# Kernel tuning notes

Hardware: AMD Instinct MI355X
Metric: run time of the kernel (lower is better)

## Reference

```python
import jax, jax.numpy as jnp
import numpy as np

VIEW_NUM = 360
CHAN_NUM = 512
BATCH = 2
IMG = 512


def setup_inputs() -> dict:
    key = jax.random.key(0)
    x = jax.random.normal(key, (BATCH, 1, IMG, IMG), dtype=jnp.float32)
    return {"x": x}


def _bilinear_sample_zeros(img, ix, iy):
    """Bilinear sample img (B,1,H,W) at pixel coords ix, iy (H,W), zeros padding.
    Matches F.grid_sample(mode='bilinear', padding_mode='zeros', align_corners=False)."""
    H, W = img.shape[-2], img.shape[-1]
    x0 = jnp.floor(ix)
    y0 = jnp.floor(iy)
    x1 = x0 + 1.0
    y1 = y0 + 1.0
    wx1 = ix - x0
    wx0 = 1.0 - wx1
    wy1 = iy - y0
    wy0 = 1.0 - wy1

    def gather(yy, xx):
        valid = (xx >= 0) & (xx <= W - 1) & (yy >= 0) & (yy <= H - 1)
        xi = jnp.clip(xx, 0, W - 1).astype(jnp.int32)
        yi = jnp.clip(yy, 0, H - 1).astype(jnp.int32)
        # fancy-index over spatial dims -> (B,1,H,W)
        return img[:, :, yi, xi] * valid.astype(img.dtype)

    return (gather(y0, x0) * (wy0 * wx0)
            + gather(y0, x1) * (wy0 * wx1)
            + gather(y1, x0) * (wy1 * wx0)
            + gather(y1, x1) * (wy1 * wx1))


def _fp(x):
    B, C, H, W = x.shape
    # affine_grid base coords, align_corners=False: (2i+1)/N - 1
    bx = (2.0 * jnp.arange(W, dtype=x.dtype) + 1.0) / W - 1.0
    by = (2.0 * jnp.arange(H, dtype=x.dtype) + 1.0) / H - 1.0
    X = bx[None, :]  # (1,W)
    Y = by[:, None]  # (H,1)
    i = jnp.arange(VIEW_NUM, dtype=x.dtype)
    angles = -jnp.pi * (i + 1.0) / VIEW_NUM - jnp.pi
    cosv = jnp.cos(angles)
    sinv = jnp.sin(angles)

    def per_view(carry, cs):
        c, s = cs
        # theta = [[c,-s,0],[s,c,0]]; grid = base @ theta^T
        gx = c * X - s * Y  # (H,W) normalized sample x
        gy = s * X + c * Y  # (H,W) normalized sample y
        # unnormalize (align_corners=False)
        ix = ((gx + 1.0) * W - 1.0) * 0.5
        iy = ((gy + 1.0) * H - 1.0) * 0.5
        samp = _bilinear_sample_zeros(x, ix, iy)  # (B,1,H,W)
        return carry, jnp.sum(samp, axis=2)  # sum over height -> (B,1,W)

    _, cols = jax.lax.scan(per_view, 0, (cosv, sinv))  # (V,B,1,W)
    sino = jnp.transpose(cols, (1, 2, 3, 0)) * 0.5  # (B,1,chanNum,viewNum)
    return sino


def reference(x):
    return _fp(x)
```

## Files before the change

kernel.cpp:

```cpp
#include <hip/hip_runtime.h>

typedef __fp16 h2 __attribute__((ext_vector_type(2)));

constexpr int VIEWS = 360;
constexpr int IMGSZ = 512;
constexpr int WCHUNK = 64;
constexpr int KH = 40;
constexpr int NXF4 = 25;
constexpr int PITCH = 100;
constexpr int MAXNY = 79;
constexpr int LDSDW = PITCH * MAXNY;
constexpr int PW = 712;
constexpr int PH = 704;
constexpr int PAD = 96;

#define ASYNC_CP16(SRC, DST)                                              \
    __builtin_amdgcn_global_load_lds(                                     \
        (const __attribute__((address_space(1))) unsigned*)(SRC),         \
        (__attribute__((address_space(3))) unsigned*)(DST), 16, 0, 0)

__global__ __launch_bounds__(256) void pad_kernel(const float* __restrict__ x,
                                                  unsigned* __restrict__ padq) {
    constexpr int PW4 = PW / 4;
    constexpr int total = PH * PW4;
    int idx = blockIdx.x * 256 + threadIdx.x;
    if (idx >= total) return;
    int py = idx / PW4;
    int px4 = idx - py * PW4;
    int gx = px4 * 4 - PAD;
    int gy = py - PAD;
    const float* img0 = x;
    const float* img1 = x + (size_t)IMGSZ * IMGSZ;
    float4 a = make_float4(0.f, 0.f, 0.f, 0.f);
    float4 bq = a;
    if ((unsigned)gy < (unsigned)IMGSZ && (unsigned)gx < (unsigned)IMGSZ) {
        size_t off = (size_t)gy * IMGSZ + gx;
        a  = *(const float4*)(img0 + off);
        bq = *(const float4*)(img1 + off);
    }
    uint4 d;
    d.x = __builtin_bit_cast(unsigned, __builtin_amdgcn_cvt_pkrtz(a.x, bq.x));
    d.y = __builtin_bit_cast(unsigned, __builtin_amdgcn_cvt_pkrtz(a.y, bq.y));
    d.z = __builtin_bit_cast(unsigned, __builtin_amdgcn_cvt_pkrtz(a.z, bq.z));
    d.w = __builtin_bit_cast(unsigned, __builtin_amdgcn_cvt_pkrtz(a.w, bq.w));
    *(uint4*)&padq[(size_t)idx * 4] = d;
}

__global__ __launch_bounds__(256) void fp_kernel(const unsigned* __restrict__ padq,
                                                 float* __restrict__ out) {
    __shared__ __align__(16) unsigned tileU[LDSDW];

    int blk = blockIdx.x;
    int wc = blk & 7;
    int v = blk >> 3;

    int tid = threadIdx.x;
    int lane = tid & 63;
    int g = tid >> 6;
    int w = wc * WCHUNK + lane;

    double ang = -3.14159265358979323846 * (double)(v + 1) / (double)VIEWS
                 - 3.14159265358979323846;
    float c = (float)cos(ang);
    float s = (float)sin(ang);

    float xw = (float)w + 0.5f - 256.0f;
    float cxw = fmaf(c, xw, 255.5f);
    float sxw = fmaf(s, xw, 255.5f);

    float lo = -1e30f, hi = 1e30f;
    {
        float coef = -s, base = cxw;
        if (fabsf(coef) > 1e-6f) {
            float a = (-1.0f - base) / coef;
            float bq = (512.0f - base) / coef;
            lo = fmaxf(lo, fminf(a, bq));
            hi = fminf(hi, fmaxf(a, bq));
        } else if (!(base > -1.0f && base < 512.0f)) {
            lo = 1e30f; hi = -1e30f;
        }
    }
    {
        float coef = c, base = sxw;
        if (fabsf(coef) > 1e-6f) {
            float a = (-1.0f - base) / coef;
            float bq = (512.0f - base) / coef;
            lo = fmaxf(lo, fminf(a, bq));
            hi = fminf(hi, fmaxf(a, bq));
        } else if (!(base > -1.0f && base < 512.0f)) {
            lo = 1e30f; hi = -1e30f;
        }
    }
    float h0f = fminf(fmaxf(floorf(lo + 255.5f) - 1.0f, 0.0f), 512.0f);
    float h1f = fminf(fmaxf(ceilf(hi + 255.5f) + 1.0f, -1.0f), 511.0f);
    int h0 = (int)h0f;
    int h1 = (int)h1f;

    int bh0 = h0, bh1 = h1;
    #pragma unroll
    for (int m = 1; m < 64; m <<= 1) {
        bh0 = min(bh0, __shfl_xor(bh0, m, 64));
        bh1 = max(bh1, __shfl_xor(bh1, m, 64));
    }

    float xa = (float)(wc * WCHUNK) + 0.5f - 256.0f;
    float xb = xa + 63.0f;

    float acc0 = 0.0f, acc1 = 0.0f;
    float step4x = -4.0f * s;
    float step4y = 4.0f * c;

    for (int hc = bh0; hc <= bh1; hc += KH) {
        int hend = min(hc + KH - 1, bh1);

        float ha = (float)hc - 255.5f;
        float hb = (float)hend - 255.5f;
        float ix00 = c * xa - s * ha, ix01 = c * xa - s * hb;
        float ix10 = c * xb - s * ha, ix11 = c * xb - s * hb;
        float iy00 = s * xa + c * ha, iy01 = s * xa + c * hb;
        float iy10 = s * xb + c * ha, iy11 = s * xb + c * hb;
        float ixmn = fminf(fminf(ix00, ix01), fminf(ix10, ix11)) + 255.5f;
        float iymn = fminf(fminf(iy00, iy01), fminf(iy10, iy11)) + 255.5f;
        float iymx = fmaxf(fmaxf(iy00, iy01), fmaxf(iy10, iy11)) + 255.5f;
        int x_lo = (int)floorf(ixmn) - 1;
        int x_lo4 = x_lo & ~3;
        int y_lo = (int)floorf(iymn) - 1;
        int NY = min((int)floorf(iymx) + 3 - y_lo, MAXNY);
        int total4 = NY * NXF4;
        int nit = (total4 + 255) >> 8;

        __syncthreads();

        {
            const unsigned* pb = padq + (y_lo + PAD) * PW + (x_lo4 + PAD);
            for (int k = 0; k < nit; ++k) {
                int i = (k << 8) + tid;
                if (((k << 8) + (g << 6) + 63) < total4) {
                    int ry = i / NXF4;
                    ASYNC_CP16(pb + 4 * i + (PW - 4 * NXF4) * ry, &tileU[i << 2]);
                } else if (i < total4) {
                    int ry = i / NXF4;
                    uint4 val = *(const uint4*)(pb + 4 * i + (PW - 4 * NXF4) * ry);
                    *(uint4*)&tileU[i << 2] = val;
                }
            }
        }
        asm volatile("s_waitcnt vmcnt(0)" ::: "memory");
        __syncthreads();

        float hh0 = (float)(hc + g) - 255.5f;
        float ixr = fmaf(-s, hh0, cxw) - (float)x_lo4;
        float iyr = fmaf(c, hh0, sxw) - (float)y_lo;
        h2 accp0 = (h2)0.0f;
        h2 accp1 = (h2)0.0f;
        int parity = 0;
        #pragma unroll 8
        for (int h = hc + g; h <= hend; h += 4) {
            float fx = floorf(ixr);
            float fy = floorf(iyr);
            int lx = (int)fx;
            int ly = (int)fy;
            float wx1 = ixr - fx;
            float wy1 = iyr - fy;
            h2 wxs = __builtin_amdgcn_cvt_pkrtz(wx1, wx1);
            h2 wys = __builtin_amdgcn_cvt_pkrtz(wy1, wy1);
            const unsigned* p = tileU + (ly * PITCH + lx);
            h2 t00 = __builtin_bit_cast(h2, p[0]);
            h2 t01 = __builtin_bit_cast(h2, p[1]);
            h2 t10 = __builtin_bit_cast(h2, p[PITCH]);
            h2 t11 = __builtin_bit_cast(h2, p[PITCH + 1]);
            h2 r0 = t00 + (t01 - t00) * wxs;
            h2 r1 = t10 + (t11 - t10) * wxs;
            h2 contrib = r0 + (r1 - r0) * wys;
            if (parity) accp1 += contrib; else accp0 += contrib;
            parity ^= 1;
            ixr += step4x;
            iyr += step4y;
        }
        acc0 += (float)accp0.x + (float)accp1.x;
        acc1 += (float)accp0.y + (float)accp1.y;
    }

    __syncthreads();
    tileU[(g << 6) + lane] = __float_as_uint(acc0);
    tileU[256 + (g << 6) + lane] = __float_as_uint(acc1);
    __syncthreads();
    if (g == 0) {
        float r0 = __uint_as_float(tileU[lane]) + __uint_as_float(tileU[64 + lane]) +
                   __uint_as_float(tileU[128 + lane]) + __uint_as_float(tileU[192 + lane]);
        float r1 = __uint_as_float(tileU[256 + lane]) + __uint_as_float(tileU[320 + lane]) +
                   __uint_as_float(tileU[384 + lane]) + __uint_as_float(tileU[448 + lane]);
        size_t o = (size_t)w * VIEWS + v;
        out[o] = r0 * 0.5f;
        out[(size_t)IMGSZ * VIEWS + o] = r1 * 0.5f;
    }
}

extern "C" void kernel_launch(void* const* d_in, const int* in_sizes, int n_in,
                              void* d_out, int out_size, void* d_ws, size_t ws_size,
                              hipStream_t stream) {
    const float* x = (const float*)d_in[0];
    float* out = (float*)d_out;
    unsigned* padq = (unsigned*)d_ws;

    constexpr int padTotal = PH * (PW / 4);
    pad_kernel<<<(padTotal + 255) / 256, 256, 0, stream>>>(x, padq);

    int nblocks = VIEWS * (IMGSZ / WCHUNK);
    fp_kernel<<<nblocks, 256, 0, stream>>>(padq, out);
}
```

Measured before the change: 165.8 us.

## Enlarge LDS tile to 104 rows with 512 threads and power-of-two pitch

The forward-projection kernel now loads taller image tiles (104 rows per chunk, 128-word pitch, up to 127 tile rows) and runs 512 threads per block, with 8 row phases instead of 4. Tile bounds are updated incrementally rather than recomputed from the four corners each chunk, and address math uses shifts instead of divides. The padded workspace geometry changes to match. This cuts the number of load and sync rounds per block, but the larger LDS footprint (about 65 KB) and bigger blocks can lower occupancy and may load more unused pixels per tile.

```diff
diff --git a/kernel.cpp b/kernel.cpp
--- a/kernel.cpp
+++ b/kernel.cpp
@@ -5,14 +5,15 @@
 constexpr int VIEWS = 360;
 constexpr int IMGSZ = 512;
 constexpr int WCHUNK = 64;
-constexpr int KH = 40;
-constexpr int NXF4 = 25;
-constexpr int PITCH = 100;
-constexpr int MAXNY = 79;
+constexpr int KH = 104;
+constexpr int NPH = 8;
+constexpr int PITCH = 128;
+constexpr int NXF4 = 32;
+constexpr int MAXNY = 127;
 constexpr int LDSDW = PITCH * MAXNY;
-constexpr int PW = 712;
-constexpr int PH = 704;
-constexpr int PAD = 96;
+constexpr int PW = 704;
+constexpr int PH = 705;
+constexpr int PAD = 68;
 
 #define ASYNC_CP16(SRC, DST)                                              \
     __builtin_amdgcn_global_load_lds(                                     \
@@ -46,7 +47,7 @@
     *(uint4*)&padq[(size_t)idx * 4] = d;
 }
 
-__global__ __launch_bounds__(256) void fp_kernel(const unsigned* __restrict__ padq,
+__global__ __launch_bounds__(512) void fp_kernel(const unsigned* __restrict__ padq,
                                                  float* __restrict__ out) {
     __shared__ __align__(16) unsigned tileU[LDSDW];
 
@@ -56,7 +57,7 @@
 
     int tid = threadIdx.x;
     int lane = tid & 63;
-    int g = tid >> 6;
+    int p = tid >> 6;
     int w = wc * WCHUNK + lane;
 
     double ang = -3.14159265358979323846 * (double)(v + 1) / (double)VIEWS
@@ -105,42 +106,55 @@
 
     float xa = (float)(wc * WCHUNK) + 0.5f - 256.0f;
     float xb = xa + 63.0f;
+    float cxa = c * xa, cxb = c * xb;
+    float sxa = s * xa, sxb = s * xb;
+    float xlo_pair = fminf(cxa, cxb);
+    float ylo_pair = fminf(sxa, sxb);
+    float yhi_pair = fmaxf(sxa, sxb);
 
     float acc0 = 0.0f, acc1 = 0.0f;
-    float step4x = -4.0f * s;
-    float step4y = 4.0f * c;
+    float step8x = -8.0f * s;
+    float step8y = 8.0f * c;
+
+    float ixmn = 0.f, iymn = 0.f, iymx = 0.f;
+    bool have = false;
 
     for (int hc = bh0; hc <= bh1; hc += KH) {
         int hend = min(hc + KH - 1, bh1);
 
-        float ha = (float)hc - 255.5f;
-        float hb = (float)hend - 255.5f;
-        float ix00 = c * xa - s * ha, ix01 = c * xa - s * hb;
-        float ix10 = c * xb - s * ha, ix11 = c * xb - s * hb;
-        float iy00 = s * xa + c * ha, iy01 = s * xa + c * hb;
-        float iy10 = s * xb + c * ha, iy11 = s * xb + c * hb;
-        float ixmn = fminf(fminf(ix00, ix01), fminf(ix10, ix11)) + 255.5f;
-        float iymn = fminf(fminf(iy00, iy01), fminf(iy10, iy11)) + 255.5f;
-        float iymx = fmaxf(fmaxf(iy00, iy01), fmaxf(iy10, iy11)) + 255.5f;
-        int x_lo = (int)floorf(ixmn) - 1;
-        int x_lo4 = x_lo & ~3;
+        if (!have || hend != hc + KH - 1) {
+            float ha = (float)hc - 255.5f;
+            float hb = (float)hend - 255.5f;
+            float sha = s * ha, shb = s * hb;
+            float cha = c * ha, chb = c * hb;
+            ixmn = xlo_pair - fmaxf(sha, shb) + 255.5f;
+            iymn = ylo_pair + fminf(cha, chb) + 255.5f;
+            iymx = yhi_pair + fmaxf(cha, chb) + 255.5f;
+        }
+        have = true;
+
+        int x_lo4 = ((int)floorf(ixmn) - 1) & ~3;
         int y_lo = (int)floorf(iymn) - 1;
         int NY = min((int)floorf(iymx) + 3 - y_lo, MAXNY);
-        int total4 = NY * NXF4;
-        int nit = (total4 + 255) >> 8;
+        int total4 = NY << 5;
+        int nit = (total4 + 511) >> 9;
+
+        ixmn -= s * (float)KH;
+        iymn += c * (float)KH;
+        iymx += c * (float)KH;
 
         __syncthreads();
 
         {
             const unsigned* pb = padq + (y_lo + PAD) * PW + (x_lo4 + PAD);
             for (int k = 0; k < nit; ++k) {
-                int i = (k << 8) + tid;
-                if (((k << 8) + (g << 6) + 63) < total4) {
-                    int ry = i / NXF4;
-                    ASYNC_CP16(pb + 4 * i + (PW - 4 * NXF4) * ry, &tileU[i << 2]);
+                int i = (k << 9) + tid;
+                if (((k << 9) + (p << 6) + 63) < total4) {
+                    int ry = i >> 5;
+                    ASYNC_CP16(pb + ((i & 31) << 2) + ry * PW, &tileU[i << 2]);
                 } else if (i < total4) {
-                    int ry = i / NXF4;
-                    uint4 val = *(const uint4*)(pb + 4 * i + (PW - 4 * NXF4) * ry);
+                    int ry = i >> 5;
+                    uint4 val = *(const uint4*)(pb + ((i & 31) << 2) + ry * PW);
                     *(uint4*)&tileU[i << 2] = val;
                 }
             }
@@ -148,14 +162,14 @@
         asm volatile("s_waitcnt vmcnt(0)" ::: "memory");
         __syncthreads();
 
-        float hh0 = (float)(hc + g) - 255.5f;
+        float hh0 = (float)(hc + p) - 255.5f;
         float ixr = fmaf(-s, hh0, cxw) - (float)x_lo4;
         float iyr = fmaf(c, hh0, sxw) - (float)y_lo;
         h2 accp0 = (h2)0.0f;
         h2 accp1 = (h2)0.0f;
         int parity = 0;
         #pragma unroll 8
-        for (int h = hc + g; h <= hend; h += 4) {
+        for (int h = hc + p; h <= hend; h += 8) {
             float fx = floorf(ixr);
             float fy = floorf(iyr);
             int lx = (int)fx;
@@ -164,35 +178,34 @@
             float wy1 = iyr - fy;
             h2 wxs = __builtin_amdgcn_cvt_pkrtz(wx1, wx1);
             h2 wys = __builtin_amdgcn_cvt_pkrtz(wy1, wy1);
-            const unsigned* p = tileU + (ly * PITCH + lx);
-            h2 t00 = __builtin_bit_cast(h2, p[0]);
-            h2 t01 = __builtin_bit_cast(h2, p[1]);
-            h2 t10 = __builtin_bit_cast(h2, p[PITCH]);
-            h2 t11 = __builtin_bit_cast(h2, p[PITCH + 1]);
+            const unsigned* pt = tileU + ((ly << 7) + lx);
+            h2 t00 = __builtin_bit_cast(h2, pt[0]);
+            h2 t01 = __builtin_bit_cast(h2, pt[1]);
+            h2 t10 = __builtin_bit_cast(h2, pt[PITCH]);
+            h2 t11 = __builtin_bit_cast(h2, pt[PITCH + 1]);
             h2 r0 = t00 + (t01 - t00) * wxs;
             h2 r1 = t10 + (t11 - t10) * wxs;
             h2 contrib = r0 + (r1 - r0) * wys;
             if (parity) accp1 += contrib; else accp0 += contrib;
             parity ^= 1;
-            ixr += step4x;
-            iyr += step4y;
+            ixr += step8x;
+            iyr += step8y;
         }
         acc0 += (float)accp0.x + (float)accp1.x;
         acc1 += (float)accp0.y + (float)accp1.y;
     }
 
     __syncthreads();
-    tileU[(g << 6) + lane] = __float_as_uint(acc0);
-    tileU[256 + (g << 6) + lane] = __float_as_uint(acc1);
+    tileU[(p << 6) + lane] = __float_as_uint(acc0);
+    tileU[512 + (p << 6) + lane] = __float_as_uint(acc1);
     __syncthreads();
-    if (g == 0) {
-        float r0 = __uint_as_float(tileU[lane]) + __uint_as_float(tileU[64 + lane]) +
-                   __uint_as_float(tileU[128 + lane]) + __uint_as_float(tileU[192 + lane]);
-        float r1 = __uint_as_float(tileU[256 + lane]) + __uint_as_float(tileU[320 + lane]) +
-                   __uint_as_float(tileU[384 + lane]) + __uint_as_float(tileU[448 + lane]);
+    if (p < 2) {
+        const unsigned* base = tileU + (p << 9);
+        float r = 0.0f;
+        #pragma unroll
+        for (int q = 0; q < 8; ++q) r += __uint_as_float(base[(q << 6) + lane]);
         size_t o = (size_t)w * VIEWS + v;
-        out[o] = r0 * 0.5f;
-        out[(size_t)IMGSZ * VIEWS + o] = r1 * 0.5f;
+        out[o + (size_t)p * IMGSZ * VIEWS] = r * 0.5f;
     }
 }
 
@@ -207,5 +220,5 @@
     pad_kernel<<<(padTotal + 255) / 256, 256, 0, stream>>>(x, padq);
 
     int nblocks = VIEWS * (IMGSZ / WCHUNK);
-    fp_kernel<<<nblocks, 256, 0, stream>>>(padq, out);
+    fp_kernel<<<nblocks, 512, 0, stream>>>(padq, out);
 }
```

Measured after the change: 189.4 us. +14.3%, slower.
